# Performance work log

Hardware: AMD Instinct MI355X
Metric: run time of the kernel (lower is better)

Reference implementation:

```python
import jax, jax.numpy as jnp
import numpy as np

B, T, I, H, L, S = 128, 256, 256, 256, 4, 3


def _gru(x_t, w_i, b_i, b_h):
    # torch.nn.GRUCell called WITHOUT hx in the source => hidden state is 0,
    # so Whh @ 0 vanishes and only the b_hh bias contributes to the gates.
    gi = x_t @ w_i.T + b_i                      # [B, 3H]
    hh = b_h.shape[0] // 3
    i_r, i_z, i_n = gi[:, :hh], gi[:, hh:2 * hh], gi[:, 2 * hh:]
    h_r, h_z, h_n = b_h[:hh], b_h[hh:2 * hh], b_h[2 * hh:]
    r = jax.nn.sigmoid(i_r + h_r)
    z = jax.nn.sigmoid(i_z + h_z)
    n = jnp.tanh(i_n + r * h_n)
    return (1.0 - z) * n                        # + z * 0


def setup_inputs() -> dict:
    key = jax.random.key(0)
    ks = jax.random.split(key, 12)
    s = 1.0 / np.sqrt(H)
    u = lambda k, shape: jax.random.uniform(k, shape, jnp.float32, -s, s)
    return {
        "x": jax.random.normal(ks[0], (B, T, I), jnp.float32),
        "hidden": jax.random.normal(ks[1], (B, L, L), jnp.float32),
        "w_ih0": u(ks[2], (S, 3 * H, I)),      # layer-0 input weights, per split
        "b_ih0": u(ks[3], (S, 3 * H)),
        "b_hh0": u(ks[4], (S, 3 * H)),
        "w_ih": u(ks[5], (S, L - 1, 3 * H, H)),  # layers 1..L-1
        "b_ih": u(ks[6], (S, L - 1, 3 * H)),
        "b_hh": u(ks[7], (S, L - 1, 3 * H)),
        "w_lw": u(ks[8], (L, H)),              # layer_weights: Linear(H -> L)
        "b_lw": u(ks[9], (L,)),
        "w_sel": u(ks[10], (S, H + I)),        # selective_layer: Linear(H+I -> S)
        "b_sel": u(ks[11], (S,)),
    }


def reference(x, hidden, w_ih0, b_ih0, b_hh0, w_ih, b_ih, b_hh, w_lw, b_lw, w_sel, b_sel):
    Lm1 = w_ih.shape[1]

    def run_stack(x_t, cur):
        # cur is a (possibly traced) int index selecting one of S GRU stacks
        hs = [_gru(x_t, w_ih0[cur], b_ih0[cur], b_hh0[cur])]
        for l in range(Lm1):
            hs.append(_gru(hs[-1], w_ih[cur, l], b_ih[cur, l], b_hh[cur, l]))
        return jnp.stack(hs, axis=1)            # [B, L, H]

    h0 = run_stack(x[:, 0, :], 0)               # first step always uses stack 0

    def step(h, x_t):
        energy = h @ w_lw.T + b_lw              # [B, L, L]
        attn = jnp.sum(hidden * energy, axis=2) # [B, L]
        a = jax.nn.softmax(attn, axis=1)
        ctx = jnp.einsum('bl,blh->bh', a, h)    # [B, H]
        scores = jnp.concatenate([ctx, x_t], axis=1) @ w_sel.T + b_sel  # [B, S]
        cur = jnp.argmax(jnp.sum(scores, axis=0))  # batch-summed routing
        h_new = run_stack(x_t, cur)
        return h_new, h_new[:, -1, :]

    h_final, ys = jax.lax.scan(step, h0, jnp.swapaxes(x[:, 1:, :], 0, 1))
    outputs = jnp.concatenate([h0[:, -1:, :], jnp.swapaxes(ys, 0, 1)], axis=1)  # [B, T, H]
    return outputs, h_final[:, -1, :]
```

## Files before the change

kernel.cpp:

```cpp
#include <hip/hip_runtime.h>
#include <math.h>

#define Bsz 128
#define Tsz 256
#define Isz 256
#define Hsz 256
#define Lsz 4
#define Ssz 3
#define Mrows (Bsz*Tsz)

using f16x8 = __attribute__((ext_vector_type(8))) _Float16;
using f32x4 = __attribute__((ext_vector_type(4))) float;

#define LOG2E 1.44269504f

__global__ __launch_bounds__(256) void f32_to_f16_3(
    const float* __restrict__ s0, _Float16* __restrict__ d0, int n0,
    const float* __restrict__ s1, _Float16* __restrict__ d1, int n1,
    const float* __restrict__ s2, _Float16* __restrict__ d2, int n2)
{
  int idx = blockIdx.x * 256 + threadIdx.x;
  const float* s; _Float16* d;
  if (idx < n0)           { s = s0; d = d0; }
  else if (idx < n0 + n1) { idx -= n0; s = s1; d = d1; }
  else                    { idx -= n0 + n1; if (idx >= n2) return; s = s2; d = d2; }
  const float4 v0 = *(const float4*)(s + (size_t)idx * 8);
  const float4 v1 = *(const float4*)(s + (size_t)idx * 8 + 4);
  _Float16 h[8];
  h[0] = (_Float16)v0.x; h[1] = (_Float16)v0.y;
  h[2] = (_Float16)v0.z; h[3] = (_Float16)v0.w;
  h[4] = (_Float16)v1.x; h[5] = (_Float16)v1.y;
  h[6] = (_Float16)v1.z; h[7] = (_Float16)v1.w;
  *(uint4*)(d + (size_t)idx * 8) = *(uint4*)h;
}

__global__ __launch_bounds__(256, 2) void gemm_gru_f16(
    const _Float16* __restrict__ Abase, size_t a_cur_stride,
    const _Float16* __restrict__ Wbase, size_t w_cur_stride,
    const float* __restrict__ bi_g, size_t bi_stride,
    const float* __restrict__ bh_g, size_t bh_stride,
    _Float16* __restrict__ Hout)
{
  __shared__ _Float16 AhS[3][8192];

  const int tid  = threadIdx.x;
  const int cu   = blockIdx.z;
  const int n0   = blockIdx.y * 64;
  const int rmb  = blockIdx.x * 512;

  const _Float16* A = Abase + (size_t)cu * a_cur_stride;
  const _Float16* W = Wbase + (size_t)cu * w_cur_stride;
  const float* bi = bi_g + (size_t)cu * bi_stride;
  const float* bh = bh_g + (size_t)cu * bh_stride;

  const int lane = tid & 63;
  const int wv   = tid >> 6;
  const int q    = lane >> 4;
  const int c    = lane & 15;

  const int ncol = n0 + wv * 16 + c;
  f16x8 wf[3][8];
  #pragma unroll
  for (int s = 0; s < 3; s++)
    #pragma unroll
    for (int k0 = 0; k0 < 8; k0++)
      wf[s][k0] = *(const f16x8*)(W + (size_t)(s * 256 + ncol) * 256 + k0 * 32 + q * 8);
  #pragma unroll
  for (int s = 0; s < 3; s++)
    #pragma unroll
    for (int k0 = 0; k0 < 8; k0++)
      asm volatile("" : "+v"(wf[s][k0]));

  const float c0  = -LOG2E * (bi[ncol] + bh[ncol]);
  const float c1  =  LOG2E * (bi[256 + ncol] + bh[256 + ncol]);
  const float c3  = 2.f * LOG2E * bi[512 + ncol];
  const float bhn = bh[512 + ncol];

  f32x4 acc[3][2];

  auto stage = [&](int buf, int ch) {
    const int rm = rmb + ch * 32;
    #pragma unroll
    for (int i = 0; i < 4; i++) {
      const int p0 = 8 * wv + 2 * i;
      const int pk = p0 + (lane >> 5);
      const _Float16* src = A + (size_t)(rm + (lane & 31)) * 256 + pk * 8;
      __builtin_amdgcn_global_load_lds(
          (const __attribute__((address_space(1))) void*)src,
          (__attribute__((address_space(3))) void*)&AhS[buf][p0 * 256],
          16, 0, 0);
    }
  };

  auto compute_chunk = [&](int buf, int ch) {
    const int rm = rmb + ch * 32;
    #pragma unroll
    for (int s = 0; s < 3; s++)
      #pragma unroll
      for (int mi = 0; mi < 2; mi++)
        acc[s][mi] = (f32x4)0.f;
    #pragma unroll
    for (int k0 = 0; k0 < 8; k0++) {
      const f16x8 a0 = *(const f16x8*)&AhS[buf][(k0 * 4 + q) * 256 + c * 8];
      const f16x8 a1 = *(const f16x8*)&AhS[buf][(k0 * 4 + q) * 256 + 128 + c * 8];
      #pragma unroll
      for (int s = 0; s < 3; s++) {
        acc[s][0] = __builtin_amdgcn_mfma_f32_16x16x32_f16(a0, wf[s][k0], acc[s][0], 0, 0, 0);
        acc[s][1] = __builtin_amdgcn_mfma_f32_16x16x32_f16(a1, wf[s][k0], acc[s][1], 0, 0, 0);
      }
    }
    #pragma unroll
    for (int mi = 0; mi < 2; mi++) {
      #pragma unroll
      for (int reg = 0; reg < 4; reg++) {
        const float ar = acc[0][mi][reg];
        const float az = acc[1][mi][reg];
        const float an = acc[2][mi][reg];
        const float e0 = __builtin_amdgcn_exp2f(fmaf(-LOG2E, ar, c0));
        const float r  = __builtin_amdgcn_rcpf(1.f + e0);
        const float e1 = __builtin_amdgcn_exp2f(fmaf(LOG2E, az, c1));
        const float tt = fmaf(r, bhn, an);
        const float a2 = fminf(fmaf(2.f * LOG2E, tt, c3), 120.f);
        const float e2 = __builtin_amdgcn_exp2f(a2);
        const float out = (e2 - 1.f) *
            __builtin_amdgcn_rcpf((1.f + e1) * (1.f + e2));
        const size_t row = (size_t)cu * Mrows + rm + mi * 16 + q * 4 + reg;
        Hout[row * 256 + ncol] = (_Float16)out;
      }
    }
  };

  stage(0, 0);
  stage(1, 1);
  asm volatile("s_waitcnt vmcnt(4)" ::: "memory");
  __builtin_amdgcn_s_barrier();

  int bc = 0;
  for (int t = 0; t < 14; ++t) {
    int bs = bc + 2; if (bs >= 3) bs -= 3;
    stage(bs, t + 2);
    compute_chunk(bc, t);
    asm volatile("s_waitcnt vmcnt(12)" ::: "memory");
    __builtin_amdgcn_s_barrier();
    bc = (bc + 1 == 3) ? 0 : bc + 1;
  }
  compute_chunk(bc, 14);
  asm volatile("s_waitcnt vmcnt(0)" ::: "memory");
  __builtin_amdgcn_s_barrier();
  bc = (bc + 1 == 3) ? 0 : bc + 1;
  compute_chunk(bc, 15);
}

__global__ __launch_bounds__(256) void ep_tile(
    const _Float16* __restrict__ Hh,
    const float* __restrict__ w_lw, const float* __restrict__ w_sel, int layer,
    float* __restrict__ e, float* __restrict__ p)
{
  __shared__ float wc[7][256];
  __shared__ float ps[4][64][8];
  const int tid = threadIdx.x;
  const size_t mg0 = (size_t)blockIdx.x * 64;

  #pragma unroll
  for (int j = 0; j < 7; j++)
    wc[j][tid] = (j < 4) ? w_lw[j * 256 + tid] : w_sel[(j - 4) * 512 + tid];
  __syncthreads();

  const int r = tid & 63, pp = tid >> 6;
  const _Float16* hrow = Hh + (mg0 + r) * 256 + pp * 64;
  float acc[7] = {0.f, 0.f, 0.f, 0.f, 0.f, 0.f, 0.f};
  #pragma unroll
  for (int i = 0; i < 8; i++) {
    union { uint4 u; _Float16 h[8]; } hv;
    hv.u = *(const uint4*)(hrow + i * 8);
    float hf[8];
    #pragma unroll
    for (int k = 0; k < 8; k++) hf[k] = (float)hv.h[k];
    #pragma unroll
    for (int j = 0; j < 7; j++) {
      const float4 w0 = *(const float4*)&wc[j][pp * 64 + i * 8];
      const float4 w1 = *(const float4*)&wc[j][pp * 64 + i * 8 + 4];
      acc[j] += hf[0] * w0.x + hf[1] * w0.y + hf[2] * w0.z + hf[3] * w0.w
              + hf[4] * w1.x + hf[5] * w1.y + hf[6] * w1.z + hf[7] * w1.w;
    }
  }
  #pragma unroll
  for (int j = 0; j < 7; j++) ps[pp][r][j] = acc[j];
  __syncthreads();

  if (tid < 64) {
    float d[7];
    #pragma unroll
    for (int j = 0; j < 7; j++)
      d[j] = ps[0][tid][j] + ps[1][tid][j] + ps[2][tid][j] + ps[3][tid][j];
    const size_t mg = mg0 + tid;
    const int cc = (int)(mg >> 15);
    const int m  = (int)(mg & 32767);
    const int b = m >> 8, t = m & 255;
    const size_t base = ((size_t)cc * Tsz + t) * Bsz + b;
    #pragma unroll
    for (int j = 0; j < 4; j++) e[base * 16 + layer * 4 + j] = d[j];
    #pragma unroll
    for (int j = 0; j < 3; j++) p[base * 12 + layer * 3 + j] = d[4 + j];
  }
}

__global__ __launch_bounds__(128) void attn_finish(
    const float* __restrict__ e, const float* __restrict__ p,
    const float* __restrict__ hidden, const float* __restrict__ b_lw,
    float* __restrict__ score_h)
{
  const int t = blockIdx.x, cc = blockIdx.y;
  const int b = threadIdx.x;
  const float* eb = e + ((size_t)(cc * Tsz + t) * Bsz + b) * 16;
  const float* pb = p + ((size_t)(cc * Tsz + t) * Bsz + b) * 12;
  const float* hb = hidden + b * 16;
  const float bl0 = b_lw[0], bl1 = b_lw[1], bl2 = b_lw[2], bl3 = b_lw[3];
  float attn[4];
  #pragma unroll
  for (int i = 0; i < 4; i++) {
    attn[i] = hb[i * 4 + 0] * (eb[i * 4 + 0] + bl0)
            + hb[i * 4 + 1] * (eb[i * 4 + 1] + bl1)
            + hb[i * 4 + 2] * (eb[i * 4 + 2] + bl2)
            + hb[i * 4 + 3] * (eb[i * 4 + 3] + bl3);
  }
  const float mx = fmaxf(fmaxf(attn[0], attn[1]), fmaxf(attn[2], attn[3]));
  float ex[4], sum = 0.f;
  #pragma unroll
  for (int i = 0; i < 4; i++) { ex[i] = expf(attn[i] - mx); sum += ex[i]; }
  const float inv = 1.f / sum;
  float sc[3];
  #pragma unroll
  for (int s = 0; s < 3; s++) {
    float v = 0.f;
    #pragma unroll
    for (int i = 0; i < 4; i++) v += ex[i] * pb[i * 3 + s];
    sc[s] = v * inv;
  }
  #pragma unroll
  for (int off = 32; off; off >>= 1)
    #pragma unroll
    for (int s = 0; s < 3; s++) sc[s] += __shfl_xor(sc[s], off);
  __shared__ float red[2][3];
  const int wv = threadIdx.x >> 6, ln = threadIdx.x & 63;
  if (ln == 0) { red[wv][0] = sc[0]; red[wv][1] = sc[1]; red[wv][2] = sc[2]; }
  __syncthreads();
  if (threadIdx.x == 0) {
    #pragma unroll
    for (int s = 0; s < 3; s++)
      score_h[((size_t)cc * Tsz + t) * 3 + s] = red[0][s] + red[1][s];
  }
}

__global__ __launch_bounds__(256) void xs_kernel(
    const float* __restrict__ x, const float* __restrict__ w_sel,
    const float* __restrict__ b_sel, float* __restrict__ xs)
{
  const int t = blockIdx.x, k = threadIdx.x;
  float s = 0.f;
  for (int b = 0; b < Bsz; b++) s += x[((size_t)b * Tsz + t) * Isz + k];
  float pr[3];
  #pragma unroll
  for (int qq = 0; qq < 3; qq++) pr[qq] = s * w_sel[qq * (Hsz + Isz) + Hsz + k];
  #pragma unroll
  for (int off = 32; off; off >>= 1)
    #pragma unroll
    for (int qq = 0; qq < 3; qq++) pr[qq] += __shfl_xor(pr[qq], off);
  __shared__ float red[4][3];
  const int wv = k >> 6, ln = k & 63;
  if (ln == 0) { red[wv][0] = pr[0]; red[wv][1] = pr[1]; red[wv][2] = pr[2]; }
  __syncthreads();
  if (k == 0) {
    #pragma unroll
    for (int qq = 0; qq < 3; qq++)
      xs[t * 3 + qq] = red[0][qq] + red[1][qq] + red[2][qq] + red[3][qq]
                      + (float)Bsz * b_sel[qq];
  }
}

__global__ __launch_bounds__(256) void select_kernel(
    const float* __restrict__ score_h, const float* __restrict__ xs,
    int* __restrict__ cur)
{
  __shared__ int f[Tsz][3];
  const int tid = threadIdx.x;
  for (int u = tid; u < (Tsz - 1) * 3; u += 256) {
    const int t = 1 + u / 3, cc = u % 3;
    const float* sh = score_h + ((size_t)cc * Tsz + (t - 1)) * 3;
    const float* xr = xs + t * 3;
    const float v0 = sh[0] + xr[0];
    const float v1 = sh[1] + xr[1];
    const float v2 = sh[2] + xr[2];
    int best = 0; float bv = v0;
    if (v1 > bv) { bv = v1; best = 1; }
    if (v2 > bv) { bv = v2; best = 2; }
    f[t][cc] = best;
  }
  __syncthreads();
  if (tid == 0) {
    int cc = 0; cur[0] = 0;
    for (int t = 1; t < Tsz; t++) { cc = f[t][cc]; cur[t] = cc; }
  }
}

__global__ __launch_bounds__(256) void gather_out(
    const _Float16* __restrict__ Hh, const int* __restrict__ cur,
    float* __restrict__ out)
{
  const size_t idx = ((size_t)blockIdx.x * 256 + threadIdx.x) * 4;
  const size_t BTH = (size_t)Bsz * Tsz * Hsz;
  int b, t, h;
  if (idx < BTH) {
    b = (int)(idx >> 16);
    const int rem = (int)(idx & 65535);
    t = rem >> 8; h = rem & 255;
  } else {
    const size_t r2 = idx - BTH;
    b = (int)(r2 >> 8); h = (int)(r2 & 255); t = Tsz - 1;
  }
  const int cc = cur[t];
  const size_t g = (((size_t)cc * Mrows + (size_t)b * Tsz + t) * Hsz + h);
  union { ushort4 u; _Float16 hv[4]; } cv;
  cv.u = *(const ushort4*)(Hh + g);
  float4 v;
  v.x = (float)cv.hv[0]; v.y = (float)cv.hv[1];
  v.z = (float)cv.hv[2]; v.w = (float)cv.hv[3];
  *(float4*)(out + idx) = v;
}

extern "C" void kernel_launch(void* const* d_in, const int* in_sizes, int n_in,
                              void* d_out, int out_size, void* d_ws, size_t ws_size,
                              hipStream_t stream) {
  const float* x      = (const float*)d_in[0];
  const float* hidden = (const float*)d_in[1];
  const float* w_ih0  = (const float*)d_in[2];
  const float* b_ih0  = (const float*)d_in[3];
  const float* b_hh0  = (const float*)d_in[4];
  const float* w_ih   = (const float*)d_in[5];
  const float* b_ih   = (const float*)d_in[6];
  const float* b_hh   = (const float*)d_in[7];
  const float* w_lw   = (const float*)d_in[8];
  const float* b_lw   = (const float*)d_in[9];
  const float* w_sel  = (const float*)d_in[10];
  const float* b_sel  = (const float*)d_in[11];
  float* out = (float*)d_out;

  char* w = (char*)d_ws;
  const size_t HN = (size_t)3 * Mrows * 256;
  const size_t XN = (size_t)Bsz * Tsz * Isz;
  const size_t W0N = (size_t)3 * 768 * 256;
  const size_t WLN = (size_t)3 * 3 * 768 * 256;
  _Float16* HA  = (_Float16*)w; w += HN * 2;
  _Float16* HB  = (_Float16*)w; w += HN * 2;
  _Float16* xh  = (_Float16*)w; w += XN * 2;
  _Float16* Wh0 = (_Float16*)w; w += W0N * 2;
  _Float16* WhL = (_Float16*)w; w += WLN * 2;
  float* e       = (float*)w; w += (size_t)3 * Tsz * Bsz * 16 * 4;
  float* p       = (float*)w; w += (size_t)3 * Tsz * Bsz * 12 * 4;
  float* score_h = (float*)w; w += (size_t)3 * Tsz * 3 * 4;
  float* xsb     = (float*)w; w += (size_t)Tsz * 3 * 4;
  int*   curb    = (int*)w;   w += (size_t)Tsz * 4;

  f32_to_f16_3<<<5248, 256, 0, stream>>>(
      x, xh, (int)(XN / 8),
      w_ih0, Wh0, (int)(W0N / 8),
      w_ih, WhL, (int)(WLN / 8));

  dim3 ggrid(64, 4, 3);

  gemm_gru_f16<<<ggrid, 256, 0, stream>>>(
      xh, (size_t)0, Wh0, (size_t)768 * 256,
      b_ih0, (size_t)768, b_hh0, (size_t)768, HA);
  ep_tile<<<(3 * Mrows) / 64, 256, 0, stream>>>(HA, w_lw, w_sel, 0, e, p);

  const size_t wcur = (size_t)3 * 768 * 256;
  const size_t bst  = (size_t)3 * 768;
  _Float16* ping = HA; _Float16* pong = HB;
  for (int l = 1; l < 4; l++) {
    gemm_gru_f16<<<ggrid, 256, 0, stream>>>(
        ping, (size_t)Mrows * 256,
        WhL + (size_t)(l - 1) * 768 * 256, wcur,
        b_ih + (size_t)(l - 1) * 768, bst,
        b_hh + (size_t)(l - 1) * 768, bst, pong);
    ep_tile<<<(3 * Mrows) / 64, 256, 0, stream>>>(pong, w_lw, w_sel, l, e, p);
    _Float16* t1 = ping; ping = pong; pong = t1;
  }

  attn_finish<<<dim3(Tsz, 3), 128, 0, stream>>>(e, p, hidden, b_lw, score_h);
  xs_kernel<<<Tsz, 256, 0, stream>>>(x, w_sel, b_sel, xsb);
  select_kernel<<<1, 256, 0, stream>>>(score_h, xsb, curb);
  gather_out<<<8224, 256, 0, stream>>>(ping, curb, out);
}
```

Baseline: 410.2 us.

## Halve GEMM row tile to double grid, parallelize routing selection with prefix scan

The GRU GEMM kernel now covers 256 rows per block instead of 512 and the grid doubles to 128 blocks in x, so there are more workgroups to spread across CUs, at the cost of reloading the per-block weight fragments twice as often. The select kernel swaps its serial single-thread chain over timesteps for a parallel prefix scan that composes 3-state transition maps packed into bitfields. This removes a 255-step serial loop, though that kernel is small relative to the GEMMs. The pipeline tail now hard-codes buffer index 1 for the last chunk; that matches the rotation for 8 chunks.

```diff
diff --git a/kernel.cpp b/kernel.cpp
--- a/kernel.cpp
+++ b/kernel.cpp
@@ -46,7 +46,7 @@
   const int tid  = threadIdx.x;
   const int cu   = blockIdx.z;
   const int n0   = blockIdx.y * 64;
-  const int rmb  = blockIdx.x * 512;
+  const int rmb  = blockIdx.x * 256;
 
   const _Float16* A = Abase + (size_t)cu * a_cur_stride;
   const _Float16* W = Wbase + (size_t)cu * w_cur_stride;
@@ -136,7 +136,7 @@
   __builtin_amdgcn_s_barrier();
 
   int bc = 0;
-  for (int t = 0; t < 14; ++t) {
+  for (int t = 0; t < 6; ++t) {
     int bs = bc + 2; if (bs >= 3) bs -= 3;
     stage(bs, t + 2);
     compute_chunk(bc, t);
@@ -144,11 +144,10 @@
     __builtin_amdgcn_s_barrier();
     bc = (bc + 1 == 3) ? 0 : bc + 1;
   }
-  compute_chunk(bc, 14);
+  compute_chunk(bc, 6);
   asm volatile("s_waitcnt vmcnt(0)" ::: "memory");
   __builtin_amdgcn_s_barrier();
-  bc = (bc + 1 == 3) ? 0 : bc + 1;
-  compute_chunk(bc, 15);
+  compute_chunk(1, 7);
 }
 
 __global__ __launch_bounds__(256) void ep_tile(
@@ -282,25 +281,44 @@
     const float* __restrict__ score_h, const float* __restrict__ xs,
     int* __restrict__ cur)
 {
-  __shared__ int f[Tsz][3];
-  const int tid = threadIdx.x;
-  for (int u = tid; u < (Tsz - 1) * 3; u += 256) {
-    const int t = 1 + u / 3, cc = u % 3;
-    const float* sh = score_h + ((size_t)cc * Tsz + (t - 1)) * 3;
+  __shared__ unsigned S[Tsz];
+  const int t = threadIdx.x;
+
+  unsigned m = 0x24;
+  if (t >= 1) {
+    m = 0;
     const float* xr = xs + t * 3;
-    const float v0 = sh[0] + xr[0];
-    const float v1 = sh[1] + xr[1];
-    const float v2 = sh[2] + xr[2];
-    int best = 0; float bv = v0;
-    if (v1 > bv) { bv = v1; best = 1; }
-    if (v2 > bv) { bv = v2; best = 2; }
-    f[t][cc] = best;
-  }
+    #pragma unroll
+    for (int cc = 0; cc < 3; cc++) {
+      const float* sh = score_h + ((size_t)cc * Tsz + (t - 1)) * 3;
+      const float v0 = sh[0] + xr[0];
+      const float v1 = sh[1] + xr[1];
+      const float v2 = sh[2] + xr[2];
+      unsigned best = 0; float bv = v0;
+      if (v1 > bv) { bv = v1; best = 1; }
+      if (v2 > bv) { bv = v2; best = 2; }
+      m |= best << (2 * cc);
+    }
+  }
+  S[t] = m;
   __syncthreads();
-  if (tid == 0) {
-    int cc = 0; cur[0] = 0;
-    for (int t = 1; t < Tsz; t++) { cc = f[t][cc]; cur[t] = cc; }
-  }
+
+  #pragma unroll
+  for (int d = 1; d < Tsz; d <<= 1) {
+    const unsigned prev = (t >= d) ? S[t - d] : 0x24u;
+    const unsigned self = S[t];
+    __syncthreads();
+    unsigned comp = 0;
+    #pragma unroll
+    for (int x = 0; x < 3; x++) {
+      const unsigned y = (prev >> (2 * x)) & 3u;
+      const unsigned z = (self >> (2 * y)) & 3u;
+      comp |= z << (2 * x);
+    }
+    S[t] = comp;
+    __syncthreads();
+  }
+  cur[t] = (int)(S[t] & 3u);
 }
 
 __global__ __launch_bounds__(256) void gather_out(
@@ -366,7 +384,7 @@
       w_ih0, Wh0, (int)(W0N / 8),
       w_ih, WhL, (int)(WLN / 8));
 
-  dim3 ggrid(64, 4, 3);
+  dim3 ggrid(128, 4, 3);
 
   gemm_gru_f16<<<ggrid, 256, 0, stream>>>(
       xh, (size_t)0, Wh0, (size_t)768 * 256,
```

Measured after the change: 417.6 us. No clear change (+1.8%).
